# Kernel tuning notes

Measured on AMD Instinct MI355X. Metric: run time of the kernel, lower is better.

## Reference

```python
import jax, jax.numpy as jnp
import numpy as np
import math

D_MODEL, NHEAD, D_FF = 1024, 16, 4096
B, S = 8, 1024
D_K = D_MODEL // NHEAD
EPS = 1e-5


def _layer_norm(x, g, b):
    m = jnp.mean(x, axis=-1, keepdims=True)
    v = jnp.mean(jnp.square(x - m), axis=-1, keepdims=True)
    return (x - m) * jax.lax.rsqrt(v + EPS) * g + b


def setup_inputs() -> dict:
    key = jax.random.key(0)
    ks = jax.random.split(key, 12)
    w = 0.02  # weight scale for numerical sanity
    d, f = D_MODEL, D_FF
    return {
        "x": jax.random.normal(ks[0], (B, S, d), jnp.float32),
        "Wq": jax.random.normal(ks[1], (d, d), jnp.float32) * w, "bq": jnp.zeros((d,), jnp.float32),
        "Wk": jax.random.normal(ks[2], (d, d), jnp.float32) * w, "bk": jnp.zeros((d,), jnp.float32),
        "Wv": jax.random.normal(ks[3], (d, d), jnp.float32) * w, "bv": jnp.zeros((d,), jnp.float32),
        "Wo": jax.random.normal(ks[4], (d, d), jnp.float32) * w, "bo": jnp.zeros((d,), jnp.float32),
        "conv_w": jax.random.normal(ks[5], (d, 3), jnp.float32) * w, "conv_b": jnp.zeros((d,), jnp.float32),
        "lna_g": jnp.ones((d,), jnp.float32), "lna_b": jnp.zeros((d,), jnp.float32),
        "W1": jax.random.normal(ks[6], (d, f), jnp.float32) * w, "b1": jnp.zeros((f,), jnp.float32),
        "W2": jax.random.normal(ks[7], (f, f), jnp.float32) * w, "b2": jnp.zeros((f,), jnp.float32),
        "W3": jax.random.normal(ks[8], (f, d), jnp.float32) * w, "b3": jnp.zeros((d,), jnp.float32),
        "Wg": jax.random.normal(ks[9], (d, d), jnp.float32) * w, "bg": jnp.zeros((d,), jnp.float32),
        "n1_g": jnp.ones((d,), jnp.float32), "n1_b": jnp.zeros((d,), jnp.float32),
        "n2_g": jnp.ones((d,), jnp.float32), "n2_b": jnp.zeros((d,), jnp.float32),
    }


def _forward(x, Wq, bq, Wk, bk, Wv, bv, Wo, bo, conv_w, conv_b, lna_g, lna_b,
             W1, b1, W2, b2, W3, b3, Wg, bg, n1_g, n1_b, n2_g, n2_b):
    b_, s_, d = x.shape
    # --- MultiScaleAttention (eval mode: dropout = identity) ---
    q = (x @ Wq + bq).reshape(b_, s_, NHEAD, D_K).transpose(0, 2, 1, 3)  # [B,H,S,Dk]
    k = (x @ Wk + bk).reshape(b_, s_, NHEAD, D_K).transpose(0, 2, 1, 3)
    v = (x @ Wv + bv).reshape(b_, s_, NHEAD, D_K).transpose(0, 2, 1, 3)
    scores = jnp.einsum('bhqd,bhkd->bhqk', q, k) / math.sqrt(D_K)
    attn = jax.nn.softmax(scores, axis=-1)
    glob = jnp.einsum('bhqk,bhkd->bhqd', attn, v).transpose(0, 2, 1, 3).reshape(b_, s_, d)
    glob = glob @ Wo + bo
    # depthwise conv1d, k=3, pad=1, over seq dim
    xp = jnp.pad(x, ((0, 0), (1, 1), (0, 0)))
    local = (xp[:, :-2] * conv_w[:, 0] + xp[:, 1:-1] * conv_w[:, 1]
             + xp[:, 2:] * conv_w[:, 2] + conv_b)
    attn_out = _layer_norm(x + glob + 0.3 * local, lna_g, lna_b)
    # --- layer body ---
    h = _layer_norm(x + attn_out, n1_g, n1_b)
    ffn = jax.nn.gelu(h @ W1 + b1, approximate=False)
    ffn = jax.nn.gelu(ffn @ W2 + b2, approximate=False)
    ffn = ffn @ W3 + b3
    gate = jax.nn.sigmoid(h @ Wg + bg)
    out = _layer_norm(h + ffn * gate, n2_g, n2_b)
    return out


def reference(x, Wq, bq, Wk, bk, Wv, bv, Wo, bo, conv_w, conv_b, lna_g, lna_b,
              W1, b1, W2, b2, W3, b3, Wg, bg, n1_g, n1_b, n2_g, n2_b):
    return _forward(x, Wq, bq, Wk, bk, Wv, bv, Wo, bo, conv_w, conv_b, lna_g, lna_b,
                    W1, b1, W2, b2, W3, b3, Wg, bg, n1_g, n1_b, n2_g, n2_b)
```

## Files before the change

kernel.cpp:

```cpp
#include <hip/hip_runtime.h>
#include <hip/hip_bf16.h>

typedef unsigned short u16;
typedef __bf16 bf16x8 __attribute__((ext_vector_type(8)));
typedef float floatx4 __attribute__((ext_vector_type(4)));
typedef __attribute__((address_space(3))) const char* lds_cp;

#define MFMA16(a, b, c) __builtin_amdgcn_mfma_f32_16x16x32_bf16((a), (b), (c), 0, 0, 0)

__device__ __forceinline__ u16 f2bf(float f) {
  __bf16 h = (__bf16)f;
  return __builtin_bit_cast(u16, h);
}
__device__ __forceinline__ float bf2f(u16 v) {
  unsigned int u = ((unsigned int)v) << 16;
  return __builtin_bit_cast(float, u);
}

__device__ __forceinline__ void async_copy16(const void* g, void* l) {
  __builtin_amdgcn_global_load_lds(
      (const __attribute__((address_space(1))) unsigned int*)g,
      (__attribute__((address_space(3))) unsigned int*)l, 16, 0, 0);
}

__device__ __forceinline__ bf16x8 ds_read16(lds_cp p) {
  bf16x8 r;
  asm volatile("ds_read_b128 %0, %1" : "=v"(r) : "v"(p));
  return r;
}
template <int IMM>
__device__ __forceinline__ bf16x8 ds_read16o(lds_cp p) {
  bf16x8 r;
  asm volatile("ds_read_b128 %0, %1 offset:%2" : "=v"(r) : "v"(p), "i"(IMM));
  return r;
}

__global__ void sentinel_k(float* out, float v) {
  if (threadIdx.x == 0 && blockIdx.x == 0) out[0] = v;
}

__global__ __launch_bounds__(256) void cast_k(const float* __restrict__ in,
                                              u16* __restrict__ out, size_t n) {
  size_t i = ((size_t)blockIdx.x * 256 + threadIdx.x) * 8;
  if (i >= n) return;
  float4 a = *(const float4*)&in[i];
  float4 b = *(const float4*)&in[i + 4];
  union { u16 q[8]; uint4 u; } pk;
  pk.q[0] = f2bf(a.x); pk.q[1] = f2bf(a.y); pk.q[2] = f2bf(a.z); pk.q[3] = f2bf(a.w);
  pk.q[4] = f2bf(b.x); pk.q[5] = f2bf(b.y); pk.q[6] = f2bf(b.z); pk.q[7] = f2bf(b.w);
  *(uint4*)&out[i] = pk.u;
}

__device__ __forceinline__ void tcast_body(const float* __restrict__ W,
                                           u16* __restrict__ Wt, int K, int N,
                                           int bx, int by, int tid) {
  __shared__ __align__(16) u16 T[64][72];
  const int k0 = bx * 64, n0 = by * 64;
  const int r = tid >> 2, cg = (tid & 3) * 16;
#pragma unroll
  for (int j = 0; j < 4; ++j) {
    float4 w = *(const float4*)&W[(size_t)(k0 + r) * N + n0 + cg + j * 4];
    union { u16 q[4]; uint2 u; } pk;
    pk.q[0] = f2bf(w.x); pk.q[1] = f2bf(w.y); pk.q[2] = f2bf(w.z); pk.q[3] = f2bf(w.w);
    *(uint2*)&T[r][cg + j * 4] = pk.u;
  }
  __syncthreads();
  const int n = tid >> 2, kg = (tid & 3) * 16;
#pragma unroll
  for (int j = 0; j < 4; ++j) {
    union { u16 q[4]; uint2 u; } pk;
#pragma unroll
    for (int i = 0; i < 4; ++i) pk.q[i] = T[kg + j * 4 + i][n];
    *(uint2*)&Wt[(size_t)(n0 + n) * K + k0 + kg + j * 4] = pk.u;
  }
}

__global__ __launch_bounds__(256) void tcast_k(const float* __restrict__ W,
                                               u16* __restrict__ Wt, int K, int N) {
  tcast_body(W, Wt, K, N, blockIdx.x, blockIdx.y, threadIdx.x);
}

__global__ __launch_bounds__(256) void tcast5_k(
    const float* __restrict__ s0, const float* __restrict__ s1,
    const float* __restrict__ s2, const float* __restrict__ s3,
    const float* __restrict__ s4, u16* __restrict__ d0, u16* __restrict__ d1,
    u16* __restrict__ d2, u16* __restrict__ d3, u16* __restrict__ d4) {
  const float* W;
  u16* Wt;
  switch (blockIdx.z) {
    case 0: W = s0; Wt = d0; break;
    case 1: W = s1; Wt = d1; break;
    case 2: W = s2; Wt = d2; break;
    case 3: W = s3; Wt = d3; break;
    default: W = s4; Wt = d4; break;
  }
  tcast_body(W, Wt, 1024, 1024, blockIdx.x, blockIdx.y, threadIdx.x);
}

__global__ __launch_bounds__(256) void catbias_k(const float* __restrict__ a,
                                                 const float* __restrict__ b,
                                                 const float* __restrict__ c,
                                                 float* __restrict__ o) {
  int i = blockIdx.x * 256 + threadIdx.x;
  if (i >= 3072) return;
  o[i] = i < 1024 ? a[i] : (i < 2048 ? b[i - 1024] : c[i - 2048]);
}

__global__ __launch_bounds__(256) void tv_k(const u16* __restrict__ V,
                                            u16* __restrict__ Vt, int VS) {
  __shared__ __align__(16) u16 T[64][72];
  const int bh = blockIdx.x, st = blockIdx.y;
  const int b = bh >> 4, h = bh & 15;
  const int s0 = st * 64;
  const int tid = threadIdx.x;
  const int r = tid >> 2, cg = (tid & 3) * 16;
#pragma unroll
  for (int j = 0; j < 2; ++j) {
    uint4 v = *(const uint4*)&V[(size_t)(b * 1024 + s0 + r) * VS + h * 64 + cg + j * 8];
    *(uint4*)&T[r][cg + j * 8] = v;
  }
  __syncthreads();
  const int dk = tid >> 2, sg = (tid & 3) * 16;
#pragma unroll
  for (int j = 0; j < 2; ++j) {
    union { u16 q[8]; uint4 u; } pk;
#pragma unroll
    for (int i = 0; i < 8; ++i) pk.q[i] = T[sg + j * 8 + i][dk];
    *(uint4*)&Vt[(size_t)(bh * 64 + dk) * 1024 + s0 + sg + j * 8] = pk.u;
  }
}

#define LDA4(dst, P, KH, MB)                                          \
  dst[0] = ds_read16o<((MB) + 0) * 1024 + (KH) * 16384 + (P) * 32768>(aB); \
  dst[1] = ds_read16o<((MB) + 1) * 1024 + (KH) * 16384 + (P) * 32768>(aB); \
  dst[2] = ds_read16o<((MB) + 2) * 1024 + (KH) * 16384 + (P) * 32768>(aB); \
  dst[3] = ds_read16o<((MB) + 3) * 1024 + (KH) * 16384 + (P) * 32768>(aB);

#define LDB4(dst, P, KH)                                              \
  dst[0] = ds_read16o<0 * 1024 + (KH) * 16384 + (P) * 32768>(bB);     \
  dst[1] = ds_read16o<1 * 1024 + (KH) * 16384 + (P) * 32768>(bB);     \
  dst[2] = ds_read16o<2 * 1024 + (KH) * 16384 + (P) * 32768>(bB);     \
  dst[3] = ds_read16o<3 * 1024 + (KH) * 16384 + (P) * 32768>(bB);

#define FENCE_MFMA()                        \
  __builtin_amdgcn_s_barrier();             \
  asm volatile("s_waitcnt lgkmcnt(0)");     \
  __builtin_amdgcn_sched_barrier(0);

#define GEMM8_TILE(P)                                                     \
  {                                                                       \
    const int t1 = (t + 1 < NT) ? t + 1 : t + 1 - NT;                     \
    const int t2 = (t + 2 < NT) ? t + 2 : t + 2 - NT;                     \
    bf16x8 a[4], b0[4], b1[4];                                            \
                                               \
    LDA4(a, P, 0, 0); LDB4(b0, P, 0);                                     \
    stA(t1, 1, (P) ^ 1);                                                  \
    FENCE_MFMA();                                                         \
    mma(a, b0, 0);                                                        \
    __builtin_amdgcn_s_barrier();                                         \
                                               \
    LDA4(a, P, 1, 0); LDB4(b1, P, 1);                                     \
    stB(t2, 0, P);                                                        \
    FENCE_MFMA();                                                         \
    mma(a, b1, 0);                                                        \
    __builtin_amdgcn_s_barrier();                                         \
                                   \
    LDA4(a, P, 0, 4);                                                     \
    stB(t2, 1, P);                                                        \
    FENCE_MFMA();                                                         \
    mma(a, b0, 4);                                                        \
    __builtin_amdgcn_s_barrier();                                         \
             \
    LDA4(a, P, 1, 4);                                                     \
    stA(t2, 0, P);                                                        \
    asm volatile("s_waitcnt vmcnt(6)");                                   \
    FENCE_MFMA();                                                         \
    mma(a, b1, 4);                                                        \
    __builtin_amdgcn_s_barrier();                                         \
  }

template <int NF, int ACT, int OBF>
__global__ __launch_bounds__(512, 2) void gemm8_k(const u16* __restrict__ A,
                                                  const u16* __restrict__ Bt,
                                                  const float* __restrict__ bias,
                                                  void* __restrict__ Cout,
                                                  int M, int N, int K, float scale) {
  static_assert(NF == 4, "gemm8_k tuned for NF=4 only");
  __shared__ __align__(16) u16 As[2][2][256 * 32];
  __shared__ __align__(16) u16 Bs[2][2][256 * 32];

  const int tid = threadIdx.x;
  const int lane = tid & 63, wv = tid >> 6;
  const int wm = wv >> 2, wn = wv & 3;
  const int g = lane >> 4, li = lane & 15;
  const int m0 = blockIdx.x * 256, n0 = blockIdx.y * 256;
  const int NT = K >> 6;

  const int srow = lane >> 2;
  const int sk8 = (lane & 3) ^ ((srow >> 1) & 3);
  const size_t abase = (size_t)(m0 + wv * 32 + srow) * K + sk8 * 8;
  const size_t bbase = (size_t)(n0 + wv * 32 + srow) * K + sk8 * 8;

  auto stA = [&](int tt, int kh, int p) {
#pragma unroll
    for (int j = 0; j < 2; ++j)
      async_copy16(A + abase + (size_t)j * 16 * K + tt * 64 + kh * 32,
                   (char*)&As[p][kh][0] + (wv * 2 + j) * 1024);
  };
  auto stB = [&](int tt, int kh, int p) {
#pragma unroll
    for (int j = 0; j < 2; ++j)
      async_copy16(Bt + bbase + (size_t)j * 16 * K + tt * 64 + kh * 32,
                   (char*)&Bs[p][kh][0] + (wv * 2 + j) * 1024);
  };

  const int swz = ((li >> 1) & 3) << 4;
  lds_cp aB = (lds_cp)((const char*)&As[0][0][0] +
                       (((wm * 128 + li) * 64 + g * 16) ^ swz));
  lds_cp bB = (lds_cp)((const char*)&Bs[0][0][0] +
                       (((wn * 64 + li) * 64 + g * 16) ^ swz));

  floatx4 acc[8][4] = {};
  auto mma = [&](bf16x8 (&a)[4], bf16x8 (&b)[4], int mb) {
    __builtin_amdgcn_s_setprio(1);
#pragma unroll
    for (int mf = 0; mf < 4; ++mf)
#pragma unroll
      for (int nf = 0; nf < 4; ++nf)
        acc[mb + mf][nf] = MFMA16(a[mf], b[nf], acc[mb + mf][nf]);
    __builtin_amdgcn_s_setprio(0);
  };

  stB(0, 0, 0); stB(0, 1, 0); stA(0, 0, 0); stA(0, 1, 0);
  stB(1, 0, 1); stB(1, 1, 1); stA(1, 0, 1);
  asm volatile("s_waitcnt vmcnt(6)");
  __builtin_amdgcn_s_barrier();

  for (int tb = 0; tb < NT; tb += 2) {
    { const int t = tb;     GEMM8_TILE(0); }
    { const int t = tb + 1; GEMM8_TILE(1); }
  }
  asm volatile("s_waitcnt vmcnt(0)");

  float bv[4];
#pragma unroll
  for (int nf = 0; nf < 4; ++nf) bv[nf] = bias[n0 + wn * 64 + nf * 16 + li];
#pragma unroll
  for (int mf = 0; mf < 8; ++mf)
#pragma unroll
    for (int nf = 0; nf < 4; ++nf)
#pragma unroll
      for (int i = 0; i < 4; ++i) {
        size_t r = (size_t)m0 + wm * 128 + mf * 16 + g * 4 + i;
        size_t c = (size_t)n0 + wn * 64 + nf * 16 + li;
        float v = (acc[mf][nf][i] + bv[nf]) * scale;
        if (ACT == 1) v = 0.5f * v * (1.0f + erff(v * 0.70710678118654752f));
        if (ACT == 2) v = 1.0f / (1.0f + __expf(-v));
        if (OBF)
          ((u16*)Cout)[r * N + c] = f2bf(v);
        else
          ((float*)Cout)[r * N + c] = v;
      }
}

template <int ACT, int OBF>
__global__ __launch_bounds__(256) void gemm_k(const u16* __restrict__ A,
                                              const u16* __restrict__ Bt,
                                              const float* __restrict__ bias,
                                              void* __restrict__ Cout, int M, int N,
                                              int K, float scale) {
  __shared__ __align__(16) u16 As[128 * 64];
  __shared__ __align__(16) u16 Bs[128 * 64];
  const int tid = threadIdx.x;
  const int lane = tid & 63;
  const int wv = tid >> 6;
  const int m0 = blockIdx.x * 128, n0 = blockIdx.y * 128;
  const int wm = (wv >> 1) * 64, wn = (wv & 1) * 64;

  floatx4 acc[4][4] = {};
  const u16* Ab = A + (size_t)m0 * K;
  const u16* Bb = Bt + (size_t)n0 * K;

  int a_off[4][2], b_off[4][2];
#pragma unroll
  for (int f = 0; f < 4; ++f) {
#pragma unroll
    for (int ks = 0; ks < 2; ++ks) {
      int kk = ks * 32 + ((lane >> 4) << 3);
      int ra = wm + f * 16 + (lane & 15);
      a_off[f][ks] = (ra * 128 + kk * 2) ^ ((ra & 7) << 4);
      int rb = wn + f * 16 + (lane & 15);
      b_off[f][ks] = (rb * 128 + kk * 2) ^ ((rb & 7) << 4);
    }
  }

  for (int kt = 0; kt < K; kt += 64) {
    __syncthreads();
#pragma unroll
    for (int it = 0; it < 4; ++it) {
      int d = it * 256 + tid;
      int row = d >> 3;
      int cgrp = ((d & 7) ^ (row & 7)) << 3;
      async_copy16(Ab + (size_t)row * K + kt + cgrp, (char*)As + (it * 256 + wv * 64) * 16);
      async_copy16(Bb + (size_t)row * K + kt + cgrp, (char*)Bs + (it * 256 + wv * 64) * 16);
    }
    __syncthreads();

    bf16x8 af[4][2], bfr[4][2];
#pragma unroll
    for (int f = 0; f < 4; ++f) {
      af[f][0] = *(const bf16x8*)((const char*)As + a_off[f][0]);
      af[f][1] = *(const bf16x8*)((const char*)As + a_off[f][1]);
      bfr[f][0] = *(const bf16x8*)((const char*)Bs + b_off[f][0]);
      bfr[f][1] = *(const bf16x8*)((const char*)Bs + b_off[f][1]);
    }
#pragma unroll
    for (int mi = 0; mi < 4; ++mi) {
#pragma unroll
      for (int ni = 0; ni < 4; ++ni) {
        acc[mi][ni] = MFMA16(af[mi][0], bfr[ni][0], acc[mi][ni]);
        acc[mi][ni] = MFMA16(af[mi][1], bfr[ni][1], acc[mi][ni]);
      }
    }
  }

  float bv[4];
#pragma unroll
  for (int ni = 0; ni < 4; ++ni) bv[ni] = bias[n0 + wn + ni * 16 + (lane & 15)];
#pragma unroll
  for (int mi = 0; mi < 4; ++mi) {
#pragma unroll
    for (int ni = 0; ni < 4; ++ni) {
#pragma unroll
      for (int i = 0; i < 4; ++i) {
        size_t r = (size_t)m0 + wm + mi * 16 + ((lane >> 4) << 2) + i;
        size_t c = (size_t)n0 + wn + ni * 16 + (lane & 15);
        float v = (acc[mi][ni][i] + bv[ni]) * scale;
        if (ACT == 1) v = 0.5f * v * (1.0f + erff(v * 0.70710678118654752f));
        if (ACT == 2) v = 1.0f / (1.0f + __expf(-v));
        if (OBF)
          ((u16*)Cout)[r * N + c] = f2bf(v);
        else
          ((float*)Cout)[r * N + c] = v;
      }
    }
  }
}

__global__ __launch_bounds__(256) void attn_k(const u16* __restrict__ Q,
                                              const u16* __restrict__ Kb,
                                              const u16* __restrict__ Vt,
                                              u16* __restrict__ Ob, int QS) {
  __shared__ __align__(16) u16 Ks[2][64 * 64];
  __shared__ __align__(16) u16 Vs[2][64 * 64];
  __shared__ __align__(16) u16 Pl[4][2048];
  const int qt = blockIdx.x, bh = blockIdx.y;
  const int b = bh >> 4, h = bh & 15;
  const int tid = threadIdx.x;
  const int lane = tid & 63, wv = tid >> 6;
  const int g = lane >> 4, li = lane & 15;
  const float SC = 0.125f * 1.4426950408889634f;

  bf16x8 qf[2][2];
#pragma unroll
  for (int m = 0; m < 2; ++m) {
    int qrow = qt * 128 + wv * 32 + m * 16 + li;
    const u16* qp = Q + ((size_t)(b * 1024 + qrow)) * QS + h * 64 + g * 8;
    qf[m][0] = *(const bf16x8*)qp;
    qf[m][1] = *(const bf16x8*)(qp + 32);
  }

  float l_i[2][4] = {};
  floatx4 o[2][4] = {};

  const int r0 = tid >> 3;
  const int csrc = ((tid & 7) ^ (r0 & 7)) * 8;
  const u16* Kg = Kb + ((size_t)b * 1024) * QS + h * 64;
  const u16* Vg = Vt + ((size_t)bh * 64) * 1024;
  char* Pw = (char*)&Pl[wv][0];

  auto stage = [&](int bi, int kv0) {
#pragma unroll
    for (int it = 0; it < 2; ++it) {
      int row = it * 32 + r0;
      async_copy16(Kg + (size_t)(kv0 + row) * QS + csrc, &Ks[bi][(it * 256 + wv * 64) * 8]);
      async_copy16(Vg + (size_t)row * 1024 + kv0 + csrc, &Vs[bi][(it * 256 + wv * 64) * 8]);
    }
  };

  stage(0, 0);
  int buf = 0;

  for (int t = 0; t < 16; ++t) {
    if (t < 15) {
      stage(buf ^ 1, (t + 1) * 64);
      asm volatile("s_waitcnt vmcnt(4)");
    } else {
      asm volatile("s_waitcnt vmcnt(0)");
    }
    __builtin_amdgcn_s_barrier();

    const char* kb = (const char*)&Ks[buf][0];
    const char* vb = (const char*)&Vs[buf][0];

    bf16x8 kf[4][2];
#pragma unroll
    for (int n = 0; n < 4; ++n) {
      int krow = n * 16 + li;
      int by0 = (krow * 128 + g * 16) ^ ((krow & 7) << 4);
      int by1 = (krow * 128 + 64 + g * 16) ^ ((krow & 7) << 4);
      kf[n][0] = ds_read16((lds_cp)kb + by0);
      kf[n][1] = ds_read16((lds_cp)kb + by1);
    }
    asm volatile("s_waitcnt lgkmcnt(0)");
    __builtin_amdgcn_sched_barrier(0);
    floatx4 s[2][4];
    __builtin_amdgcn_s_setprio(1);
#pragma unroll
    for (int m = 0; m < 2; ++m)
#pragma unroll
      for (int n = 0; n < 4; ++n) {
        floatx4 z = {0.f, 0.f, 0.f, 0.f};
        s[m][n] = MFMA16(qf[m][0], kf[n][0], z);
        s[m][n] = MFMA16(qf[m][1], kf[n][1], s[m][n]);
      }
    __builtin_amdgcn_s_setprio(0);

#pragma unroll
    for (int m = 0; m < 2; ++m) {
      float rs[4] = {0.f, 0.f, 0.f, 0.f};
#pragma unroll
      for (int n = 0; n < 4; ++n)
#pragma unroll
        for (int i = 0; i < 4; ++i) {
          float p = exp2f(s[m][n][i] * SC);
          rs[i] += p;
          int row = m * 16 + g * 4 + i, col = n * 16 + li;
          int byte = (row * 128 + col * 2) ^ ((row & 7) << 4);
          *(u16*)(Pw + byte) = f2bf(p);
        }
#pragma unroll
      for (int off = 8; off >= 1; off >>= 1)
#pragma unroll
        for (int i = 0; i < 4; ++i) rs[i] += __shfl_xor(rs[i], off);
#pragma unroll
      for (int i = 0; i < 4; ++i) l_i[m][i] += rs[i];
    }

    bf16x8 vf[4][2];
#pragma unroll
    for (int nd = 0; nd < 4; ++nd) {
      int vrow = nd * 16 + li;
      int vb0 = (vrow * 128 + g * 16) ^ ((vrow & 7) << 4);
      int vb1 = (vrow * 128 + 64 + g * 16) ^ ((vrow & 7) << 4);
      vf[nd][0] = ds_read16((lds_cp)vb + vb0);
      vf[nd][1] = ds_read16((lds_cp)vb + vb1);
    }
    bf16x8 pf[2][2];
#pragma unroll
    for (int m = 0; m < 2; ++m) {
      int prow = m * 16 + li;
      int pb0 = (prow * 128 + g * 16) ^ ((prow & 7) << 4);
      int pb1 = (prow * 128 + 64 + g * 16) ^ ((prow & 7) << 4);
      pf[m][0] = *(const bf16x8*)(Pw + pb0);
      pf[m][1] = *(const bf16x8*)(Pw + pb1);
    }
    asm volatile("s_waitcnt lgkmcnt(0)");
    __builtin_amdgcn_sched_barrier(0);
    __builtin_amdgcn_s_setprio(1);
#pragma unroll
    for (int m = 0; m < 2; ++m)
#pragma unroll
      for (int nd = 0; nd < 4; ++nd) {
        o[m][nd] = MFMA16(pf[m][0], vf[nd][0], o[m][nd]);
        o[m][nd] = MFMA16(pf[m][1], vf[nd][1], o[m][nd]);
      }
    __builtin_amdgcn_s_setprio(0);

    __builtin_amdgcn_s_barrier();
    buf ^= 1;
  }

#pragma unroll
  for (int m = 0; m < 2; ++m)
#pragma unroll
    for (int nd = 0; nd < 4; ++nd)
#pragma unroll
      for (int i = 0; i < 4; ++i) {
        size_t r = (size_t)(b * 1024 + qt * 128 + wv * 32 + m * 16 + g * 4 + i);
        Ob[r * 1024 + h * 64 + nd * 16 + li] = f2bf(o[m][nd][i] / l_i[m][i]);
      }
}

__device__ __forceinline__ void bsum2(float& a, float& b, float* sred, int tid) {
#pragma unroll
  for (int off = 32; off; off >>= 1) {
    a += __shfl_down(a, off);
    b += __shfl_down(b, off);
  }
  const int wv = tid >> 6;
  if ((tid & 63) == 0) { sred[wv] = a; sred[4 + wv] = b; }
  __syncthreads();
  a = sred[0] + sred[1] + sred[2] + sred[3];
  b = sred[4] + sred[5] + sred[6] + sred[7];
  __syncthreads();
}

__device__ __forceinline__ void ld4(const float* p, float v[4]) {
  float4 t = *(const float4*)p;
  v[0] = t.x; v[1] = t.y; v[2] = t.z; v[3] = t.w;
}
__device__ __forceinline__ void ld4bf(const u16* p, float v[4]) {
  union { uint2 u; u16 q[4]; } t;
  t.u = *(const uint2*)p;
#pragma unroll
  for (int j = 0; j < 4; ++j) v[j] = bf2f(t.q[j]);
}

__global__ __launch_bounds__(256) void post_attn_k(
    const float* __restrict__ x, const u16* __restrict__ G,
    const float* __restrict__ cw, const float* __restrict__ cb,
    const float* __restrict__ lag, const float* __restrict__ lab,
    const float* __restrict__ n1g, const float* __restrict__ n1b,
    u16* __restrict__ hb) {
  __shared__ float sred[8];
  const size_t row = blockIdx.x;
  const int s = (int)(row & 1023);
  const int tid = threadIdx.x, d = tid * 4;

  float xv[4], xm[4] = {0, 0, 0, 0}, xp[4] = {0, 0, 0, 0}, gv[4], cbv[4];
  ld4(&x[row * 1024 + d], xv);
  if (s > 0) ld4(&x[(row - 1) * 1024 + d], xm);
  if (s < 1023) ld4(&x[(row + 1) * 1024 + d], xp);
  ld4bf(&G[row * 1024 + d], gv);
  float c0[4], c1[4], c2[4];
  ld4(&cw[d * 3], c0);
  ld4(&cw[d * 3 + 4], c1);
  ld4(&cw[d * 3 + 8], c2);
  ld4(&cb[d], cbv);
  float w0[4] = {c0[0], c0[3], c1[2], c2[1]};
  float w1[4] = {c0[1], c1[0], c1[3], c2[2]};
  float w2[4] = {c0[2], c1[1], c2[0], c2[3]};

  float t[4], sa = 0.f, sb = 0.f;
#pragma unroll
  for (int j = 0; j < 4; ++j) {
    float loc = xm[j] * w0[j] + xv[j] * w1[j] + xp[j] * w2[j] + cbv[j];
    t[j] = xv[j] + gv[j] + 0.3f * loc;
    sa += t[j];
    sb += t[j] * t[j];
  }
  bsum2(sa, sb, sred, tid);
  float mean = sa * (1.f / 1024.f);
  float rstd = rsqrtf(sb * (1.f / 1024.f) - mean * mean + 1e-5f);
  float lg[4], lbv[4];
  ld4(&lag[d], lg);
  ld4(&lab[d], lbv);
  float hp[4];
  sa = 0.f; sb = 0.f;
#pragma unroll
  for (int j = 0; j < 4; ++j) {
    float a = (t[j] - mean) * rstd * lg[j] + lbv[j];
    hp[j] = xv[j] + a;
    sa += hp[j];
    sb += hp[j] * hp[j];
  }
  bsum2(sa, sb, sred, tid);
  float mean2 = sa * (1.f / 1024.f);
  float rstd2 = rsqrtf(sb * (1.f / 1024.f) - mean2 * mean2 + 1e-5f);
  float g2[4], b2[4];
  ld4(&n1g[d], g2);
  ld4(&n1b[d], b2);
  union { u16 q[4]; uint2 u; } pk;
#pragma unroll
  for (int j = 0; j < 4; ++j) pk.q[j] = f2bf((hp[j] - mean2) * rstd2 * g2[j] + b2[j]);
  *(uint2*)&hb[row * 1024 + d] = pk.u;
}

__global__ __launch_bounds__(256) void final_k(const u16* __restrict__ h,
                                               const u16* __restrict__ f3,
                                               const u16* __restrict__ gt,
                                               const float* __restrict__ n2g,
                                               const float* __restrict__ n2b,
                                               float* __restrict__ out) {
  __shared__ float sred[8];
  const size_t row = blockIdx.x;
  const int tid = threadIdx.x, d = tid * 4;
  float hv[4], fv[4], gv[4];
  ld4bf(&h[row * 1024 + d], hv);
  ld4bf(&f3[row * 1024 + d], fv);
  ld4bf(&gt[row * 1024 + d], gv);
  float t[4], sa = 0.f, sb = 0.f;
#pragma unroll
  for (int j = 0; j < 4; ++j) {
    t[j] = hv[j] + fv[j] * gv[j];
    sa += t[j];
    sb += t[j] * t[j];
  }
  bsum2(sa, sb, sred, tid);
  float mean = sa * (1.f / 1024.f);
  float rstd = rsqrtf(sb * (1.f / 1024.f) - mean * mean + 1e-5f);
  float g2[4], b2[4];
  ld4(&n2g[d], g2);
  ld4(&n2b[d], b2);
  float o[4];
#pragma unroll
  for (int j = 0; j < 4; ++j) o[j] = (t[j] - mean) * rstd * g2[j] + b2[j];
  *(float4*)&out[row * 1024 + d] = make_float4(o[0], o[1], o[2], o[3]);
}

extern "C" void kernel_launch(void* const* d_in, const int* in_sizes, int n_in,
                              void* d_out, int out_size, void* d_ws, size_t ws_size,
                              hipStream_t stream) {
  (void)in_sizes; (void)n_in; (void)out_size;
  const float* x   = (const float*)d_in[0];
  const float* Wq  = (const float*)d_in[1];
  const float* bq  = (const float*)d_in[2];
  const float* Wk  = (const float*)d_in[3];
  const float* bk  = (const float*)d_in[4];
  const float* Wv  = (const float*)d_in[5];
  const float* bv  = (const float*)d_in[6];
  const float* Wo  = (const float*)d_in[7];
  const float* bo  = (const float*)d_in[8];
  const float* cw  = (const float*)d_in[9];
  const float* cb  = (const float*)d_in[10];
  const float* lag = (const float*)d_in[11];
  const float* lab = (const float*)d_in[12];
  const float* W1  = (const float*)d_in[13];
  const float* b1  = (const float*)d_in[14];
  const float* W2  = (const float*)d_in[15];
  const float* b2  = (const float*)d_in[16];
  const float* W3  = (const float*)d_in[17];
  const float* b3  = (const float*)d_in[18];
  const float* Wg  = (const float*)d_in[19];
  const float* bg  = (const float*)d_in[20];
  const float* n1g = (const float*)d_in[21];
  const float* n1b = (const float*)d_in[22];
  const float* n2g = (const float*)d_in[23];
  const float* n2b = (const float*)d_in[24];

  const size_t MB = 1024ull * 1024ull;
  if (ws_size < 122 * MB) {
    sentinel_k<<<1, 64, 0, stream>>>((float*)d_out, (float)ws_size);
    return;
  }
  char* ws = (char*)d_ws;
  char* dob = (char*)d_out;
  u16* WoT   = (u16*)(ws + 0 * MB);
  u16* WgT   = (u16*)(ws + 2 * MB);
  u16* W1T   = (u16*)(ws + 4 * MB);
  u16* W2T   = (u16*)(ws + 12 * MB);
  u16* W3T   = (u16*)(ws + 44 * MB);
  u16* WqkvT = (u16*)(ws + 52 * MB);
  float* bqkv = (float*)(dob + 28 * MB);
  u16* xb    = (u16*)(ws + 58 * MB);
  u16* QKV   = (u16*)(ws + 74 * MB);
  u16* hb    = (u16*)(ws + 74 * MB);
  u16* f1h   = (u16*)(ws + 90 * MB);
  u16* gate  = (u16*)(ws + 90 * MB);
  u16* G     = xb;
  u16* f3    = xb;
  u16* Vt    = (u16*)dob;
  u16* globb = (u16*)(dob + 16 * MB);
  u16* f2h   = (u16*)dob;

  cast_k<<<4096, 256, 0, stream>>>(x, xb, (size_t)8192 * 1024);
  tcast5_k<<<dim3(16, 16, 5), 256, 0, stream>>>(Wq, Wk, Wv, Wo, Wg,
                                                WqkvT, WqkvT + 1024 * 1024,
                                                WqkvT + 2048 * 1024, WoT, WgT);
  tcast_k<<<dim3(16, 64), 256, 0, stream>>>(W1, W1T, 1024, 4096);
  tcast_k<<<dim3(64, 64), 256, 0, stream>>>(W2, W2T, 4096, 4096);
  tcast_k<<<dim3(64, 16), 256, 0, stream>>>(W3, W3T, 4096, 1024);
  catbias_k<<<12, 256, 0, stream>>>(bq, bk, bv, bqkv);

  gemm8_k<4, 0, 1><<<dim3(32, 12), 512, 0, stream>>>(xb, WqkvT, bqkv, QKV, 8192, 3072, 1024, 1.0f);
  tv_k<<<dim3(128, 16), 256, 0, stream>>>(QKV + 2048, Vt, 3072);
  attn_k<<<dim3(8, 128), 256, 0, stream>>>(QKV, QKV + 1024, Vt, globb, 3072);
  gemm_k<0, 1><<<dim3(64, 8), 256, 0, stream>>>(globb, WoT, bo, G, 8192, 1024, 1024, 1.0f);
  post_attn_k<<<8192, 256, 0, stream>>>(x, G, cw, cb, lag, lab, n1g, n1b, hb);

  for (int hf = 0; hf < 2; ++hf) {
    const size_t M0 = (size_t)hf * 4096;
    gemm8_k<4, 1, 1><<<dim3(16, 16), 512, 0, stream>>>(hb + M0 * 1024, W1T, b1, f1h,
                                                       4096, 4096, 1024, 1.0f);
    gemm8_k<4, 1, 1><<<dim3(16, 16), 512, 0, stream>>>(f1h, W2T, b2, f2h,
                                                       4096, 4096, 4096, 1.0f);
    gemm_k<0, 1><<<dim3(32, 8), 256, 0, stream>>>(f2h, W3T, b3, f3 + M0 * 1024,
                                                  4096, 1024, 4096, 1.0f);
  }
  gemm_k<2, 1><<<dim3(64, 8), 256, 0, stream>>>(hb, WgT, bg, gate, 8192, 1024, 1024, 1.0f);
  final_k<<<8192, 256, 0, stream>>>(hb, f3, gate, n2g, n2b, (float*)d_out);
}
```

Measured before the change: 791.8 us.

## Restructure GEMM main loop into two phases with larger fragment batches

The inner tile of the 256x256 bf16 GEMM is reorganised from four LDS-read/MFMA phases per K-tile into two. Each phase now loads both A halves (and, in the first phase, both B halves) into registers, then issues 32 MFMAs under raised priority. Global-to-LDS async copies are regrouped and the vmcnt waits are retuned to match. Launch bounds drop to one block per CU so the extra fragment registers fit. The aim is to halve the barrier and wait count per tile and give the matrix units longer uninterrupted runs, at the cost of more VGPRs and less overlap between LDS reads and MFMAs.

```diff
diff --git a/kernel.cpp b/kernel.cpp
--- a/kernel.cpp
+++ b/kernel.cpp
@@ -142,45 +142,40 @@
   dst[2] = ds_read16o<2 * 1024 + (KH) * 16384 + (P) * 32768>(bB);     \
   dst[3] = ds_read16o<3 * 1024 + (KH) * 16384 + (P) * 32768>(bB);
 
-#define FENCE_MFMA()                        \
-  __builtin_amdgcn_s_barrier();             \
-  asm volatile("s_waitcnt lgkmcnt(0)");     \
-  __builtin_amdgcn_sched_barrier(0);
-
-#define GEMM8_TILE(P)                                                     \
+#define GEMM8_TILE2(P)                                                    \
   {                                                                       \
     const int t1 = (t + 1 < NT) ? t + 1 : t + 1 - NT;                     \
     const int t2 = (t + 2 < NT) ? t + 2 : t + 2 - NT;                     \
-    bf16x8 a[4], b0[4], b1[4];                                            \
-                                               \
-    LDA4(a, P, 0, 0); LDB4(b0, P, 0);                                     \
+    bf16x8 a0[4], a1[4], b0[4], b1[4];                                    \
+               \
+    LDB4(b0, P, 0); LDB4(b1, P, 1);                                       \
+    LDA4(a0, P, 0, 0); LDA4(a1, P, 0, 4);                                 \
     stA(t1, 1, (P) ^ 1);                                                  \
-    FENCE_MFMA();                                                         \
-    mma(a, b0, 0);                                                        \
+    asm volatile("s_waitcnt vmcnt(8)");                                   \
     __builtin_amdgcn_s_barrier();                                         \
-                                               \
-    LDA4(a, P, 1, 0); LDB4(b1, P, 1);                                     \
-    stB(t2, 0, P);                                                        \
-    FENCE_MFMA();                                                         \
-    mma(a, b1, 0);                                                        \
+    asm volatile("s_waitcnt lgkmcnt(0)");                                 \
+    __builtin_amdgcn_sched_barrier(0);                                    \
+    __builtin_amdgcn_s_setprio(1);                                        \
+    mma(a0, b0, 0);                                                       \
+    mma(a1, b0, 4);                                                       \
+    __builtin_amdgcn_s_setprio(0);                                        \
     __builtin_amdgcn_s_barrier();                                         \
-                                   \
-    LDA4(a, P, 0, 4);                                                     \
-    stB(t2, 1, P);                                                        \
-    FENCE_MFMA();                                                         \
-    mma(a, b0, 4);                                                        \
+                            \
+    LDA4(a0, P, 1, 0); LDA4(a1, P, 1, 4);                                 \
+    stB(t2, 0, P); stB(t2, 1, P); stA(t2, 0, P);                          \
+    asm volatile("s_waitcnt vmcnt(8)");                                   \
     __builtin_amdgcn_s_barrier();                                         \
-             \
-    LDA4(a, P, 1, 4);                                                     \
-    stA(t2, 0, P);                                                        \
-    asm volatile("s_waitcnt vmcnt(6)");                                   \
-    FENCE_MFMA();                                                         \
-    mma(a, b1, 4);                                                        \
+    asm volatile("s_waitcnt lgkmcnt(0)");                                 \
+    __builtin_amdgcn_sched_barrier(0);                                    \
+    __builtin_amdgcn_s_setprio(1);                                        \
+    mma(a0, b1, 0);                                                       \
+    mma(a1, b1, 4);                                                       \
+    __builtin_amdgcn_s_setprio(0);                                        \
     __builtin_amdgcn_s_barrier();                                         \
   }
 
 template <int NF, int ACT, int OBF>
-__global__ __launch_bounds__(512, 2) void gemm8_k(const u16* __restrict__ A,
+__global__ __launch_bounds__(512, 1) void gemm8_k(const u16* __restrict__ A,
                                                   const u16* __restrict__ Bt,
                                                   const float* __restrict__ bias,
                                                   void* __restrict__ Cout,
@@ -222,23 +217,21 @@
 
   floatx4 acc[8][4] = {};
   auto mma = [&](bf16x8 (&a)[4], bf16x8 (&b)[4], int mb) {
-    __builtin_amdgcn_s_setprio(1);
 #pragma unroll
     for (int mf = 0; mf < 4; ++mf)
 #pragma unroll
       for (int nf = 0; nf < 4; ++nf)
         acc[mb + mf][nf] = MFMA16(a[mf], b[nf], acc[mb + mf][nf]);
-    __builtin_amdgcn_s_setprio(0);
   };
 
   stB(0, 0, 0); stB(0, 1, 0); stA(0, 0, 0); stA(0, 1, 0);
   stB(1, 0, 1); stB(1, 1, 1); stA(1, 0, 1);
-  asm volatile("s_waitcnt vmcnt(6)");
+  asm volatile("s_waitcnt vmcnt(8)");
   __builtin_amdgcn_s_barrier();
 
   for (int tb = 0; tb < NT; tb += 2) {
-    { const int t = tb;     GEMM8_TILE(0); }
-    { const int t = tb + 1; GEMM8_TILE(1); }
+    { const int t = tb;     GEMM8_TILE2(0); }
+    { const int t = tb + 1; GEMM8_TILE2(1); }
   }
   asm volatile("s_waitcnt vmcnt(0)");
 
```

Measured after the change: 829.4 us. 1.05x slower.

## Double-buffer LDS in 128x128 GEMM to overlap global loads with MFMA

Applied to the files above, without the earlier changes.

Replaces the single-buffered 128x128 GEMM with a two-stage LDS ping-pong. Tile t+2 is prefetched with async global-to-LDS copies while tile t is computed, and waits use explicit vmcnt/lgkmcnt counters plus raw barriers. It also raises wave priority around the MFMA block and sets launch bounds for two blocks per CU. The aim is to hide global load latency in the Wo, W3 and gate GEMMs. In exchange it doubles LDS use (64KB per block), which may limit occupancy. The wraparound prefetch at the end issues redundant loads.

```diff
diff --git a/kernel.cpp b/kernel.cpp
--- a/kernel.cpp
+++ b/kernel.cpp
@@ -264,18 +264,19 @@
 }
 
 template <int ACT, int OBF>
-__global__ __launch_bounds__(256) void gemm_k(const u16* __restrict__ A,
-                                              const u16* __restrict__ Bt,
-                                              const float* __restrict__ bias,
-                                              void* __restrict__ Cout, int M, int N,
-                                              int K, float scale) {
-  __shared__ __align__(16) u16 As[128 * 64];
-  __shared__ __align__(16) u16 Bs[128 * 64];
+__global__ __launch_bounds__(256, 2) void gemm2_k(const u16* __restrict__ A,
+                                                  const u16* __restrict__ Bt,
+                                                  const float* __restrict__ bias,
+                                                  void* __restrict__ Cout, int M,
+                                                  int N, int K, float scale) {
+  __shared__ __align__(16) u16 As[2][128 * 64];
+  __shared__ __align__(16) u16 Bs[2][128 * 64];
   const int tid = threadIdx.x;
   const int lane = tid & 63;
   const int wv = tid >> 6;
   const int m0 = blockIdx.x * 128, n0 = blockIdx.y * 128;
   const int wm = (wv >> 1) * 64, wn = (wv & 1) * 64;
+  const int NT = K >> 6;
 
   floatx4 acc[4][4] = {};
   const u16* Ab = A + (size_t)m0 * K;
@@ -293,27 +294,46 @@
       b_off[f][ks] = (rb * 128 + kk * 2) ^ ((rb & 7) << 4);
     }
   }
-
-  for (int kt = 0; kt < K; kt += 64) {
-    __syncthreads();
+  const int srow = tid >> 3;
+  const int scg = ((tid & 7) ^ (srow & 7)) << 3;
+
+  auto stage = [&](int tt, int p) {
 #pragma unroll
     for (int it = 0; it < 4; ++it) {
-      int d = it * 256 + tid;
-      int row = d >> 3;
-      int cgrp = ((d & 7) ^ (row & 7)) << 3;
-      async_copy16(Ab + (size_t)row * K + kt + cgrp, (char*)As + (it * 256 + wv * 64) * 16);
-      async_copy16(Bb + (size_t)row * K + kt + cgrp, (char*)Bs + (it * 256 + wv * 64) * 16);
-    }
-    __syncthreads();
+      int row = it * 32 + srow;
+      async_copy16(Ab + (size_t)row * K + tt * 64 + scg,
+                   (char*)&As[p][0] + (it * 256 + wv * 64) * 16);
+      async_copy16(Bb + (size_t)row * K + tt * 64 + scg,
+                   (char*)&Bs[p][0] + (it * 256 + wv * 64) * 16);
+    }
+  };
+
+  stage(0, 0);
+  stage(1, 1);
+  asm volatile("s_waitcnt vmcnt(8)");
+  __builtin_amdgcn_s_barrier();
+
+  for (int t = 0; t < NT; ++t) {
+    const int p = t & 1;
+    const int t2 = (t + 2 < NT) ? t + 2 : t + 2 - NT;
+    lds_cp aL = (lds_cp)(const char*)&As[p][0];
+    lds_cp bL = (lds_cp)(const char*)&Bs[p][0];
 
     bf16x8 af[4][2], bfr[4][2];
 #pragma unroll
     for (int f = 0; f < 4; ++f) {
-      af[f][0] = *(const bf16x8*)((const char*)As + a_off[f][0]);
-      af[f][1] = *(const bf16x8*)((const char*)As + a_off[f][1]);
-      bfr[f][0] = *(const bf16x8*)((const char*)Bs + b_off[f][0]);
-      bfr[f][1] = *(const bf16x8*)((const char*)Bs + b_off[f][1]);
-    }
+      af[f][0] = ds_read16(aL + a_off[f][0]);
+      af[f][1] = ds_read16(aL + a_off[f][1]);
+      bfr[f][0] = ds_read16(bL + b_off[f][0]);
+      bfr[f][1] = ds_read16(bL + b_off[f][1]);
+    }
+    asm volatile("s_waitcnt lgkmcnt(0)");
+    __builtin_amdgcn_sched_barrier(0);
+    __builtin_amdgcn_s_barrier();
+
+    stage(t2, p);
+
+    __builtin_amdgcn_s_setprio(1);
 #pragma unroll
     for (int mi = 0; mi < 4; ++mi) {
 #pragma unroll
@@ -322,7 +342,12 @@
         acc[mi][ni] = MFMA16(af[mi][1], bfr[ni][1], acc[mi][ni]);
       }
     }
-  }
+    __builtin_amdgcn_s_setprio(0);
+
+    asm volatile("s_waitcnt vmcnt(8)");
+    __builtin_amdgcn_s_barrier();
+  }
+  asm volatile("s_waitcnt vmcnt(0)");
 
   float bv[4];
 #pragma unroll
@@ -676,7 +701,7 @@
   gemm8_k<4, 0, 1><<<dim3(32, 12), 512, 0, stream>>>(xb, WqkvT, bqkv, QKV, 8192, 3072, 1024, 1.0f);
   tv_k<<<dim3(128, 16), 256, 0, stream>>>(QKV + 2048, Vt, 3072);
   attn_k<<<dim3(8, 128), 256, 0, stream>>>(QKV, QKV + 1024, Vt, globb, 3072);
-  gemm_k<0, 1><<<dim3(64, 8), 256, 0, stream>>>(globb, WoT, bo, G, 8192, 1024, 1024, 1.0f);
+  gemm2_k<0, 1><<<dim3(64, 8), 256, 0, stream>>>(globb, WoT, bo, G, 8192, 1024, 1024, 1.0f);
   post_attn_k<<<8192, 256, 0, stream>>>(x, G, cw, cb, lag, lab, n1g, n1b, hb);
 
   for (int hf = 0; hf < 2; ++hf) {
@@ -685,9 +710,9 @@
                                                        4096, 4096, 1024, 1.0f);
     gemm8_k<4, 1, 1><<<dim3(16, 16), 512, 0, stream>>>(f1h, W2T, b2, f2h,
                                                        4096, 4096, 4096, 1.0f);
-    gemm_k<0, 1><<<dim3(32, 8), 256, 0, stream>>>(f2h, W3T, b3, f3 + M0 * 1024,
-                                                  4096, 1024, 4096, 1.0f);
-  }
-  gemm_k<2, 1><<<dim3(64, 8), 256, 0, stream>>>(hb, WgT, bg, gate, 8192, 1024, 1024, 1.0f);
+    gemm2_k<0, 1><<<dim3(32, 8), 256, 0, stream>>>(f2h, W3T, b3, f3 + M0 * 1024,
+                                                   4096, 1024, 4096, 1.0f);
+  }
+  gemm2_k<2, 1><<<dim3(64, 8), 256, 0, stream>>>(hb, WgT, bg, gate, 8192, 1024, 1024, 1.0f);
   final_k<<<8192, 256, 0, stream>>>(hb, f3, gate, n2g, n2b, (float*)d_out);
 }
```

New measurement: 714.8 us. -9.7%, faster.
